# Performance work log

Hardware: AMD Instinct MI355X
Metric: run time of the kernel (lower is better)

## Reference

```python
import jax, jax.numpy as jnp
import numpy as np

B, N, C = 2048, 128, 128
H = 4
NW = 64


def setup_inputs() -> dict:
    key = jax.random.key(0)
    ks = jax.random.split(key, 6)
    return {
        "x": jax.random.normal(ks[0], (B, N, C), dtype=jnp.float32),
        "mask": jax.random.normal(ks[1], (NW, N, N), dtype=jnp.float32),
        "qkv_w": jax.random.normal(ks[2], (3 * C, C), dtype=jnp.float32) * (C ** -0.5),
        "qkv_b": jax.random.normal(ks[3], (3 * C,), dtype=jnp.float32) * 0.02,
        "proj_w": jax.random.normal(ks[4], (C, C), dtype=jnp.float32) * (C ** -0.5),
        "proj_b": jax.random.normal(ks[5], (C,), dtype=jnp.float32) * 0.02,
    }


def reference(x, mask, qkv_w, qkv_b, proj_w, proj_b):
    b, n, c = x.shape
    h = H
    hd = c // h
    scale = hd ** -0.5
    # qkv projection: [B,N,3C] -> [3,B,H,N,hd]
    qkv = (x @ qkv_w.T + qkv_b).reshape(b, n, 3, h, hd).transpose(2, 0, 3, 1, 4)
    q, k, v = qkv[0], qkv[1], qkv[2]
    # scores [B,H,N,N]
    attn = jnp.einsum("bhnd,bhmd->bhnm", q, k) * scale
    nw = mask.shape[0]
    # add per-window mask: view as [B//nW, nW, H, N, N] + mask[None,:,None]
    attn = attn.reshape(b // nw, nw, h, n, n) + mask[None, :, None, :, :]
    attn = attn.reshape(b, h, n, n)
    attn = jax.nn.softmax(attn, axis=-1)
    out = jnp.einsum("bhnm,bhmd->bhnd", attn, v)
    out = out.transpose(0, 2, 1, 3).reshape(b, n, c)
    out = out @ proj_w.T + proj_b
    return out
```

## Files before the change

### kernel.cpp

```cpp
#include <hip/hip_runtime.h>

typedef __bf16 bf16x8 __attribute__((ext_vector_type(8)));
typedef __bf16 bf16x4 __attribute__((ext_vector_type(4)));
typedef float  f32x4  __attribute__((ext_vector_type(4)));

__device__ __forceinline__ int swz(int row, int colb) {
    return row * 256 + (colb ^ ((row & 7) << 4));
}
__device__ __forceinline__ int pswz(int row, int colb) {
    return row * 128 + (colb ^ ((row & 7) << 4));
}

__global__ void prep_weights(const float* __restrict__ qkv_w,
                             const float* __restrict__ proj_w,
                             __bf16* __restrict__ wq, __bf16* __restrict__ wp) {
    int i = blockIdx.x * 256 + threadIdx.x;
    wq[i] = (__bf16)qkv_w[i];
    if (i < 16384) wp[i] = (__bf16)proj_w[i];
}

#define A_LDS_X   0
#define A_LDS_P   0
#define A_LDS_Q   32768
#define A_LDS_K   49152
#define A_LDS_VT  65536
#define A_LDS_TOTAL 81920

__global__ void __launch_bounds__(256, 2)
attn_split(const float* __restrict__ x, const float* __restrict__ mask,
           const float* __restrict__ qkv_b,
           const __bf16* __restrict__ wq,
           __bf16* __restrict__ Og) {
    extern __shared__ char smem[];
    const int b    = blockIdx.x >> 1;
    const int hp   = blockIdx.x & 1;
    const int tid  = threadIdx.x;
    const int wave = tid >> 6;
    const int lane = tid & 63;
    const int l16  = lane & 15;
    const int lg   = lane >> 4;

    {
        const float* xb = x + (size_t)b * 16384;
        #pragma unroll
        for (int it = 0; it < 8; ++it) {
            int i   = it * 256 + tid;
            int row = i >> 4;
            int c8  = (i & 15) << 3;
            float4 f0 = *(const float4*)(xb + row * 128 + c8);
            float4 f1 = *(const float4*)(xb + row * 128 + c8 + 4);
            bf16x8 v;
            v[0] = (__bf16)f0.x; v[1] = (__bf16)f0.y; v[2] = (__bf16)f0.z; v[3] = (__bf16)f0.w;
            v[4] = (__bf16)f1.x; v[5] = (__bf16)f1.y; v[6] = (__bf16)f1.z; v[7] = (__bf16)f1.w;
            *(bf16x8*)(smem + A_LDS_X + swz(row, c8 * 2)) = v;
        }
    }
    __syncthreads();

    const int f0 = wave * 48;
    #pragma unroll
    for (int pass = 0; pass < 2; ++pass) {
        f32x4 acc[3][4];
        #pragma unroll
        for (int jt = 0; jt < 3; ++jt)
            #pragma unroll
            for (int nt = 0; nt < 4; ++nt)
                acc[jt][nt] = {0.f, 0.f, 0.f, 0.f};
        int jg_t[3];
        #pragma unroll
        for (int jt = 0; jt < 3; ++jt) {
            int ft = f0 + jt * 16;
            jg_t[jt] = (ft < 64) ? (hp * 64 + ft)
                     : (ft < 128) ? (128 + hp * 64 + (ft - 64))
                                  : (256 + hp * 64 + (ft - 128));
        }
        #pragma unroll
        for (int kc = 0; kc < 4; ++kc) {
            bf16x8 afr[3];
            #pragma unroll
            for (int jt = 0; jt < 3; ++jt)
                afr[jt] = *(const bf16x8*)(wq + (jg_t[jt] + l16) * 128 + kc * 32 + lg * 8);
            bf16x8 bfr[4];
            #pragma unroll
            for (int nt = 0; nt < 4; ++nt)
                bfr[nt] = *(const bf16x8*)(smem + A_LDS_X +
                            swz((pass * 4 + nt) * 16 + l16, (kc * 32 + lg * 8) * 2));
            #pragma unroll
            for (int jt = 0; jt < 3; ++jt)
                #pragma unroll
                for (int nt = 0; nt < 4; ++nt)
                    acc[jt][nt] = __builtin_amdgcn_mfma_f32_16x16x32_bf16(
                                      afr[jt], bfr[nt], acc[jt][nt], 0, 0, 0);
        }
        #pragma unroll
        for (int jt = 0; jt < 3; ++jt) {
            int ft = f0 + jt * 16;
            int f  = ft + lg * 4;
            float4 bias = *(const float4*)(qkv_b + jg_t[jt] + lg * 4);
            #pragma unroll
            for (int nt = 0; nt < 4; ++nt) {
                int n = (pass * 4 + nt) * 16 + l16;
                f32x4 a = acc[jt][nt];
                __bf16 e0 = (__bf16)(a[0] + bias.x);
                __bf16 e1 = (__bf16)(a[1] + bias.y);
                __bf16 e2 = (__bf16)(a[2] + bias.z);
                __bf16 e3 = (__bf16)(a[3] + bias.w);
                if (f < 64) {
                    bf16x4 v4 = {e0, e1, e2, e3};
                    *(bf16x4*)(smem + A_LDS_Q + pswz(n, f * 2)) = v4;
                } else if (f < 128) {
                    bf16x4 v4 = {e0, e1, e2, e3};
                    *(bf16x4*)(smem + A_LDS_K + pswz(n, (f - 64) * 2)) = v4;
                } else {
                    int d = f - 128;
                    *(__bf16*)(smem + A_LDS_VT + swz(d + 0, n * 2)) = e0;
                    *(__bf16*)(smem + A_LDS_VT + swz(d + 1, n * 2)) = e1;
                    *(__bf16*)(smem + A_LDS_VT + swz(d + 2, n * 2)) = e2;
                    *(__bf16*)(smem + A_LDS_VT + swz(d + 3, n * 2)) = e3;
                }
            }
        }
    }
    __syncthreads();

    const int hl = wave >> 1;
    const int rh = wave & 1;
    const int hgl = hp * 2 + hl;
    const float sc = 0.17677669529663687f;
    bf16x8 kfr[8];
    #pragma unroll
    for (int mt = 0; mt < 8; ++mt)
        kfr[mt] = *(const bf16x8*)(smem + A_LDS_K +
                      pswz(mt * 16 + l16, (hl * 32 + lg * 8) * 2));
    bf16x8 vfr[2][4];
    #pragma unroll
    for (int dt = 0; dt < 2; ++dt)
        #pragma unroll
        for (int kc = 0; kc < 4; ++kc)
            vfr[dt][kc] = *(const bf16x8*)(smem + A_LDS_VT +
                            swz(hl * 32 + dt * 16 + l16, (kc * 32 + lg * 8) * 2));

    const float* mwin = mask + (size_t)(b & 63) * 16384;
    char* pbase = smem + A_LDS_P + wave * 2048;

    #pragma unroll
    for (int i = 0; i < 4; ++i) {
        const int nt = rh * 4 + i;
        bf16x8 qfr = *(const bf16x8*)(smem + A_LDS_Q +
                        pswz(nt * 16 + l16, (hl * 32 + lg * 8) * 2));
        f32x4 s[8];
        #pragma unroll
        for (int mt = 0; mt < 8; ++mt) {
            f32x4 z = {0.f, 0.f, 0.f, 0.f};
            s[mt] = __builtin_amdgcn_mfma_f32_16x16x32_bf16(qfr, kfr[mt], z, 0, 0, 0);
        }
        float mx[4] = {-1e30f, -1e30f, -1e30f, -1e30f};
        #pragma unroll
        for (int mt = 0; mt < 8; ++mt)
            #pragma unroll
            for (int r = 0; r < 4; ++r) {
                float v = s[mt][r] * sc + mwin[(nt * 16 + lg * 4 + r) * 128 + mt * 16 + l16];
                s[mt][r] = v;
                mx[r] = fmaxf(mx[r], v);
            }
        #pragma unroll
        for (int r = 0; r < 4; ++r) {
            float m = mx[r];
            m = fmaxf(m, __shfl_xor(m, 1));
            m = fmaxf(m, __shfl_xor(m, 2));
            m = fmaxf(m, __shfl_xor(m, 4));
            m = fmaxf(m, __shfl_xor(m, 8));
            mx[r] = m;
        }
        float sm[4] = {0.f, 0.f, 0.f, 0.f};
        #pragma unroll
        for (int mt = 0; mt < 8; ++mt)
            #pragma unroll
            for (int r = 0; r < 4; ++r) {
                float p = __expf(s[mt][r] - mx[r]);
                s[mt][r] = p;
                sm[r] += p;
            }
        #pragma unroll
        for (int r = 0; r < 4; ++r) {
            float t = sm[r];
            t += __shfl_xor(t, 1);
            t += __shfl_xor(t, 2);
            t += __shfl_xor(t, 4);
            t += __shfl_xor(t, 8);
            sm[r] = 1.f / t;
        }
        f32x4 o[2];
        o[0] = {0.f, 0.f, 0.f, 0.f};
        o[1] = {0.f, 0.f, 0.f, 0.f};
        #pragma unroll
        for (int hpp = 0; hpp < 2; ++hpp) {
            #pragma unroll
            for (int mtl = 0; mtl < 4; ++mtl) {
                int mt = hpp * 4 + mtl;
                #pragma unroll
                for (int r = 0; r < 4; ++r)
                    *(__bf16*)(pbase + pswz(lg * 4 + r, (mtl * 16 + l16) * 2)) =
                        (__bf16)(s[mt][r] * sm[r]);
            }
            #pragma unroll
            for (int q = 0; q < 2; ++q) {
                int kc = hpp * 2 + q;
                bf16x8 pafr = *(const bf16x8*)(pbase + pswz(l16, (q * 32 + lg * 8) * 2));
                #pragma unroll
                for (int dt = 0; dt < 2; ++dt)
                    o[dt] = __builtin_amdgcn_mfma_f32_16x16x32_bf16(
                                pafr, vfr[dt][kc], o[dt], 0, 0, 0);
            }
        }
        #pragma unroll
        for (int dt = 0; dt < 2; ++dt)
            #pragma unroll
            for (int r = 0; r < 4; ++r)
                Og[((size_t)b * 128 + nt * 16 + lg * 4 + r) * 128 +
                   hgl * 32 + dt * 16 + l16] = (__bf16)o[dt][r];
    }
}

__global__ void __launch_bounds__(256)
proj_out(const __bf16* __restrict__ Og, const __bf16* __restrict__ wp,
         const float* __restrict__ proj_b, float* __restrict__ out) {
    const int b    = blockIdx.x;
    const int tid  = threadIdx.x;
    const int wave = tid >> 6;
    const int l16  = tid & 15;
    const int lg   = (tid & 63) >> 4;

    f32x4 facc[2][8];
    #pragma unroll
    for (int nt2 = 0; nt2 < 2; ++nt2)
        #pragma unroll
        for (int ct = 0; ct < 8; ++ct)
            facc[nt2][ct] = {0.f, 0.f, 0.f, 0.f};
    #pragma unroll
    for (int kc = 0; kc < 4; ++kc) {
        bf16x8 afr[2];
        #pragma unroll
        for (int nt2 = 0; nt2 < 2; ++nt2)
            afr[nt2] = *(const bf16x8*)(Og +
                          ((size_t)b * 128 + wave * 32 + nt2 * 16 + l16) * 128 +
                          kc * 32 + lg * 8);
        bf16x8 bfr[8];
        #pragma unroll
        for (int ct = 0; ct < 8; ++ct)
            bfr[ct] = *(const bf16x8*)(wp + (ct * 16 + l16) * 128 + kc * 32 + lg * 8);
        #pragma unroll
        for (int nt2 = 0; nt2 < 2; ++nt2)
            #pragma unroll
            for (int ct = 0; ct < 8; ++ct)
                facc[nt2][ct] = __builtin_amdgcn_mfma_f32_16x16x32_bf16(
                                    afr[nt2], bfr[ct], facc[nt2][ct], 0, 0, 0);
    }
    float* ob = out + (size_t)b * 16384;
    #pragma unroll
    for (int ct = 0; ct < 8; ++ct) {
        float pb = proj_b[ct * 16 + l16];
        #pragma unroll
        for (int nt2 = 0; nt2 < 2; ++nt2) {
            int n0 = wave * 32 + nt2 * 16 + lg * 4;
            #pragma unroll
            for (int r = 0; r < 4; ++r)
                ob[(n0 + r) * 128 + ct * 16 + l16] = facc[nt2][ct][r] + pb;
        }
    }
}

#define LDS_XO 0
#define LDS_Q  32768
#define LDS_K  65536
#define LDS_VT 98304
#define LDS_P  131072
#define LDS_TOTAL 147456

__global__ void __launch_bounds__(512, 2)
attn_fused(const float* __restrict__ x, const float* __restrict__ mask,
           const float* __restrict__ qkv_b, const float* __restrict__ proj_b,
           const __bf16* __restrict__ wq, const __bf16* __restrict__ wp,
           float* __restrict__ out) {
    extern __shared__ char smem[];
    const int b    = blockIdx.x;
    const int tid  = threadIdx.x;
    const int wave = tid >> 6;
    const int lane = tid & 63;
    const int l16  = lane & 15;
    const int lg   = lane >> 4;

    {
        const float* xb = x + (size_t)b * 16384;
        #pragma unroll
        for (int it = 0; it < 4; ++it) {
            int i   = it * 512 + tid;
            int row = i >> 4;
            int c8  = (i & 15) << 3;
            float4 f0 = *(const float4*)(xb + row * 128 + c8);
            float4 f1 = *(const float4*)(xb + row * 128 + c8 + 4);
            bf16x8 v;
            v[0] = (__bf16)f0.x; v[1] = (__bf16)f0.y; v[2] = (__bf16)f0.z; v[3] = (__bf16)f0.w;
            v[4] = (__bf16)f1.x; v[5] = (__bf16)f1.y; v[6] = (__bf16)f1.z; v[7] = (__bf16)f1.w;
            *(bf16x8*)(smem + LDS_XO + swz(row, c8 * 2)) = v;
        }
    }
    __syncthreads();

    const int j0 = wave * 48;
    #pragma unroll
    for (int pass = 0; pass < 2; ++pass) {
        f32x4 acc[3][4];
        #pragma unroll
        for (int jt = 0; jt < 3; ++jt)
            #pragma unroll
            for (int nt = 0; nt < 4; ++nt)
                acc[jt][nt] = {0.f, 0.f, 0.f, 0.f};
        #pragma unroll
        for (int kc = 0; kc < 4; ++kc) {
            bf16x8 afr[3];
            #pragma unroll
            for (int jt = 0; jt < 3; ++jt)
                afr[jt] = *(const bf16x8*)(wq + (j0 + jt * 16 + l16) * 128 + kc * 32 + lg * 8);
            bf16x8 bfr[4];
            #pragma unroll
            for (int nt = 0; nt < 4; ++nt)
                bfr[nt] = *(const bf16x8*)(smem + LDS_XO +
                            swz((pass * 4 + nt) * 16 + l16, (kc * 32 + lg * 8) * 2));
            #pragma unroll
            for (int jt = 0; jt < 3; ++jt)
                #pragma unroll
                for (int nt = 0; nt < 4; ++nt)
                    acc[jt][nt] = __builtin_amdgcn_mfma_f32_16x16x32_bf16(
                                      afr[jt], bfr[nt], acc[jt][nt], 0, 0, 0);
        }
        #pragma unroll
        for (int jt = 0; jt < 3; ++jt) {
            int jbase = j0 + jt * 16 + lg * 4;
            float4 bias = *(const float4*)(qkv_b + jbase);
            #pragma unroll
            for (int nt = 0; nt < 4; ++nt) {
                int n = (pass * 4 + nt) * 16 + l16;
                f32x4 a = acc[jt][nt];
                __bf16 e0 = (__bf16)(a[0] + bias.x);
                __bf16 e1 = (__bf16)(a[1] + bias.y);
                __bf16 e2 = (__bf16)(a[2] + bias.z);
                __bf16 e3 = (__bf16)(a[3] + bias.w);
                if (jbase < 128) {
                    bf16x4 v4 = {e0, e1, e2, e3};
                    *(bf16x4*)(smem + LDS_Q + swz(n, jbase * 2)) = v4;
                } else if (jbase < 256) {
                    bf16x4 v4 = {e0, e1, e2, e3};
                    *(bf16x4*)(smem + LDS_K + swz(n, (jbase - 128) * 2)) = v4;
                } else {
                    int d = jbase - 256;
                    *(__bf16*)(smem + LDS_VT + swz(d + 0, n * 2)) = e0;
                    *(__bf16*)(smem + LDS_VT + swz(d + 1, n * 2)) = e1;
                    *(__bf16*)(smem + LDS_VT + swz(d + 2, n * 2)) = e2;
                    *(__bf16*)(smem + LDS_VT + swz(d + 3, n * 2)) = e3;
                }
            }
        }
    }
    __syncthreads();

    const int h  = wave >> 1;
    const int rh = wave & 1;
    const float sc = 0.17677669529663687f;
    bf16x8 kfr[8];
    #pragma unroll
    for (int mt = 0; mt < 8; ++mt)
        kfr[mt] = *(const bf16x8*)(smem + LDS_K + swz(mt * 16 + l16, (h * 32 + lg * 8) * 2));
    bf16x8 vfr[2][4];
    #pragma unroll
    for (int dt = 0; dt < 2; ++dt)
        #pragma unroll
        for (int kc = 0; kc < 4; ++kc)
            vfr[dt][kc] = *(const bf16x8*)(smem + LDS_VT +
                            swz(h * 32 + dt * 16 + l16, (kc * 32 + lg * 8) * 2));

    const float* mwin = mask + (size_t)(b & 63) * 16384;
    char* pbase = smem + LDS_P + wave * 2048;

    #pragma unroll
    for (int i = 0; i < 4; ++i) {
        const int nt = rh * 4 + i;
        bf16x8 qfr = *(const bf16x8*)(smem + LDS_Q + swz(nt * 16 + l16, (h * 32 + lg * 8) * 2));
        f32x4 s[8];
        #pragma unroll
        for (int mt = 0; mt < 8; ++mt) {
            f32x4 z = {0.f, 0.f, 0.f, 0.f};
            s[mt] = __builtin_amdgcn_mfma_f32_16x16x32_bf16(qfr, kfr[mt], z, 0, 0, 0);
        }
        float mx[4] = {-1e30f, -1e30f, -1e30f, -1e30f};
        #pragma unroll
        for (int mt = 0; mt < 8; ++mt)
            #pragma unroll
            for (int r = 0; r < 4; ++r) {
                float v = s[mt][r] * sc + mwin[(nt * 16 + lg * 4 + r) * 128 + mt * 16 + l16];
                s[mt][r] = v;
                mx[r] = fmaxf(mx[r], v);
            }
        #pragma unroll
        for (int r = 0; r < 4; ++r) {
            float m = mx[r];
            m = fmaxf(m, __shfl_xor(m, 1));
            m = fmaxf(m, __shfl_xor(m, 2));
            m = fmaxf(m, __shfl_xor(m, 4));
            m = fmaxf(m, __shfl_xor(m, 8));
            mx[r] = m;
        }
        float sm[4] = {0.f, 0.f, 0.f, 0.f};
        #pragma unroll
        for (int mt = 0; mt < 8; ++mt)
            #pragma unroll
            for (int r = 0; r < 4; ++r) {
                float p = __expf(s[mt][r] - mx[r]);
                s[mt][r] = p;
                sm[r] += p;
            }
        #pragma unroll
        for (int r = 0; r < 4; ++r) {
            float t = sm[r];
            t += __shfl_xor(t, 1);
            t += __shfl_xor(t, 2);
            t += __shfl_xor(t, 4);
            t += __shfl_xor(t, 8);
            sm[r] = 1.f / t;
        }
        f32x4 o[2];
        o[0] = {0.f, 0.f, 0.f, 0.f};
        o[1] = {0.f, 0.f, 0.f, 0.f};
        #pragma unroll
        for (int hp2 = 0; hp2 < 2; ++hp2) {
            #pragma unroll
            for (int mtl = 0; mtl < 4; ++mtl) {
                int mt = hp2 * 4 + mtl;
                #pragma unroll
                for (int r = 0; r < 4; ++r)
                    *(__bf16*)(pbase + pswz(lg * 4 + r, (mtl * 16 + l16) * 2)) =
                        (__bf16)(s[mt][r] * sm[r]);
            }
            #pragma unroll
            for (int q = 0; q < 2; ++q) {
                int kc = hp2 * 2 + q;
                bf16x8 pafr = *(const bf16x8*)(pbase + pswz(l16, (q * 32 + lg * 8) * 2));
                #pragma unroll
                for (int dt = 0; dt < 2; ++dt)
                    o[dt] = __builtin_amdgcn_mfma_f32_16x16x32_bf16(
                                pafr, vfr[dt][kc], o[dt], 0, 0, 0);
            }
        }
        #pragma unroll
        for (int dt = 0; dt < 2; ++dt)
            #pragma unroll
            for (int r = 0; r < 4; ++r)
                *(__bf16*)(smem + LDS_XO +
                    swz(nt * 16 + lg * 4 + r, (h * 32 + dt * 16 + l16) * 2)) = (__bf16)o[dt][r];
    }
    __syncthreads();

    f32x4 facc[8];
    #pragma unroll
    for (int ct = 0; ct < 8; ++ct)
        facc[ct] = {0.f, 0.f, 0.f, 0.f};
    #pragma unroll
    for (int kc = 0; kc < 4; ++kc) {
        bf16x8 afr = *(const bf16x8*)(smem + LDS_XO +
                        swz(wave * 16 + l16, (kc * 32 + lg * 8) * 2));
        bf16x8 bfr[8];
        #pragma unroll
        for (int ct = 0; ct < 8; ++ct)
            bfr[ct] = *(const bf16x8*)(wp + (ct * 16 + l16) * 128 + kc * 32 + lg * 8);
        #pragma unroll
        for (int ct = 0; ct < 8; ++ct)
            facc[ct] = __builtin_amdgcn_mfma_f32_16x16x32_bf16(
                           afr, bfr[ct], facc[ct], 0, 0, 0);
    }
    float* ob = out + (size_t)b * 16384;
    #pragma unroll
    for (int ct = 0; ct < 8; ++ct) {
        float pb = proj_b[ct * 16 + l16];
        int n0 = wave * 16 + lg * 4;
        #pragma unroll
        for (int r = 0; r < 4; ++r)
            ob[(n0 + r) * 128 + ct * 16 + l16] = facc[ct][r] + pb;
    }
}

extern "C" void kernel_launch(void* const* d_in, const int* in_sizes, int n_in,
                              void* d_out, int out_size, void* d_ws, size_t ws_size,
                              hipStream_t stream) {
    const float* x      = (const float*)d_in[0];
    const float* mask   = (const float*)d_in[1];
    const float* qkv_w  = (const float*)d_in[2];
    const float* qkv_b  = (const float*)d_in[3];
    const float* proj_w = (const float*)d_in[4];
    const float* proj_b = (const float*)d_in[5];
    float* out = (float*)d_out;

    __bf16* wq = (__bf16*)d_ws;
    __bf16* wp = wq + 49152;

    prep_weights<<<192, 256, 0, stream>>>(qkv_w, proj_w, wq, wp);

    const size_t og_bytes = (size_t)2048 * 128 * 128 * 2;
    const size_t need = 131072 + og_bytes;

    if (ws_size >= need) {
        __bf16* Og = (__bf16*)((char*)d_ws + 131072);
        hipFuncSetAttribute((const void*)attn_split,
                            hipFuncAttributeMaxDynamicSharedMemorySize, A_LDS_TOTAL);
        attn_split<<<4096, 256, A_LDS_TOTAL, stream>>>(x, mask, qkv_b, wq, Og);
        proj_out<<<2048, 256, 0, stream>>>(Og, wp, proj_b, out);
    } else {
        hipFuncSetAttribute((const void*)attn_fused,
                            hipFuncAttributeMaxDynamicSharedMemorySize, LDS_TOTAL);
        attn_fused<<<2048, 512, LDS_TOTAL, stream>>>(x, mask, qkv_b, proj_b, wq, wp, out);
    }
}
```

Measured before the change: 408.5 us.

## Transpose MFMA operands for vectorized mask loads and output stores

Swaps the MFMA operand order in the score, PV and output-projection matmuls so each lane holds four consecutive columns of one row. Mask loads and Og/out stores become float4/bf16x4 accesses, and the row max/sum reductions need two cross-lane shuffles instead of four per row. Softmax normalization moves from the probabilities to the PV output. The probabilities are written to a larger swizzled LDS tile (4096 bytes per wave instead of 2048), and all four PV A-fragments are read up front. This raises per-wave LDS use and changes rounding slightly, since unnormalized probabilities are cast to bf16.

```diff
diff --git a/kernel.cpp b/kernel.cpp
--- a/kernel.cpp
+++ b/kernel.cpp
@@ -141,7 +141,7 @@
                             swz(hl * 32 + dt * 16 + l16, (kc * 32 + lg * 8) * 2));
 
     const float* mwin = mask + (size_t)(b & 63) * 16384;
-    char* pbase = smem + A_LDS_P + wave * 2048;
+    char* pbase = smem + A_LDS_P + wave * 4096;
 
     #pragma unroll
     for (int i = 0; i < 4; ++i) {
@@ -152,73 +152,68 @@
         #pragma unroll
         for (int mt = 0; mt < 8; ++mt) {
             f32x4 z = {0.f, 0.f, 0.f, 0.f};
-            s[mt] = __builtin_amdgcn_mfma_f32_16x16x32_bf16(qfr, kfr[mt], z, 0, 0, 0);
-        }
-        float mx[4] = {-1e30f, -1e30f, -1e30f, -1e30f};
-        #pragma unroll
-        for (int mt = 0; mt < 8; ++mt)
+            s[mt] = __builtin_amdgcn_mfma_f32_16x16x32_bf16(kfr[mt], qfr, z, 0, 0, 0);
+        }
+        const float* mrow = mwin + (size_t)(nt * 16 + l16) * 128;
+        #pragma unroll
+        for (int mt = 0; mt < 8; ++mt) {
+            float4 mk = *(const float4*)(mrow + mt * 16 + lg * 4);
+            s[mt][0] = fmaf(s[mt][0], sc, mk.x);
+            s[mt][1] = fmaf(s[mt][1], sc, mk.y);
+            s[mt][2] = fmaf(s[mt][2], sc, mk.z);
+            s[mt][3] = fmaf(s[mt][3], sc, mk.w);
+        }
+        f32x4 vm0 = s[0], vm1 = s[1];
+        #pragma unroll
+        for (int mt = 2; mt < 8; mt += 2) { 
+            vm0[0]=fmaxf(vm0[0],s[mt][0]); vm0[1]=fmaxf(vm0[1],s[mt][1]);
+            vm0[2]=fmaxf(vm0[2],s[mt][2]); vm0[3]=fmaxf(vm0[3],s[mt][3]);
+            vm1[0]=fmaxf(vm1[0],s[mt+1][0]); vm1[1]=fmaxf(vm1[1],s[mt+1][1]);
+            vm1[2]=fmaxf(vm1[2],s[mt+1][2]); vm1[3]=fmaxf(vm1[3],s[mt+1][3]);
+        }
+        float mx = fmaxf(fmaxf(fmaxf(vm0[0],vm1[0]), fmaxf(vm0[1],vm1[1])),
+                         fmaxf(fmaxf(vm0[2],vm1[2]), fmaxf(vm0[3],vm1[3])));
+        mx = fmaxf(mx, __shfl_xor(mx, 16));
+        mx = fmaxf(mx, __shfl_xor(mx, 32));
+        f32x4 vs = {0.f, 0.f, 0.f, 0.f};
+        #pragma unroll
+        for (int mt = 0; mt < 8; ++mt) {
             #pragma unroll
             for (int r = 0; r < 4; ++r) {
-                float v = s[mt][r] * sc + mwin[(nt * 16 + lg * 4 + r) * 128 + mt * 16 + l16];
-                s[mt][r] = v;
-                mx[r] = fmaxf(mx[r], v);
-            }
-        #pragma unroll
-        for (int r = 0; r < 4; ++r) {
-            float m = mx[r];
-            m = fmaxf(m, __shfl_xor(m, 1));
-            m = fmaxf(m, __shfl_xor(m, 2));
-            m = fmaxf(m, __shfl_xor(m, 4));
-            m = fmaxf(m, __shfl_xor(m, 8));
-            mx[r] = m;
-        }
-        float sm[4] = {0.f, 0.f, 0.f, 0.f};
-        #pragma unroll
-        for (int mt = 0; mt < 8; ++mt)
-            #pragma unroll
-            for (int r = 0; r < 4; ++r) {
-                float p = __expf(s[mt][r] - mx[r]);
+                float p = __expf(s[mt][r] - mx);
                 s[mt][r] = p;
-                sm[r] += p;
-            }
-        #pragma unroll
-        for (int r = 0; r < 4; ++r) {
-            float t = sm[r];
-            t += __shfl_xor(t, 1);
-            t += __shfl_xor(t, 2);
-            t += __shfl_xor(t, 4);
-            t += __shfl_xor(t, 8);
-            sm[r] = 1.f / t;
-        }
+                vs[r] += p;
+            }
+        }
+        float sm = (vs[0] + vs[1]) + (vs[2] + vs[3]);
+        sm += __shfl_xor(sm, 16);
+        sm += __shfl_xor(sm, 32);
+        float inv = 1.f / sm;
+        #pragma unroll
+        for (int mt = 0; mt < 8; ++mt) {
+            bf16x4 pv = {(__bf16)s[mt][0], (__bf16)s[mt][1],
+                         (__bf16)s[mt][2], (__bf16)s[mt][3]};
+            *(bf16x4*)(pbase + swz(l16, mt * 32 + lg * 8)) = pv;
+        }
+        bf16x8 pafr[4];
+        #pragma unroll
+        for (int kc = 0; kc < 4; ++kc)
+            pafr[kc] = *(const bf16x8*)(pbase + swz(l16, kc * 64 + lg * 16));
         f32x4 o[2];
         o[0] = {0.f, 0.f, 0.f, 0.f};
         o[1] = {0.f, 0.f, 0.f, 0.f};
         #pragma unroll
-        for (int hpp = 0; hpp < 2; ++hpp) {
-            #pragma unroll
-            for (int mtl = 0; mtl < 4; ++mtl) {
-                int mt = hpp * 4 + mtl;
-                #pragma unroll
-                for (int r = 0; r < 4; ++r)
-                    *(__bf16*)(pbase + pswz(lg * 4 + r, (mtl * 16 + l16) * 2)) =
-                        (__bf16)(s[mt][r] * sm[r]);
-            }
-            #pragma unroll
-            for (int q = 0; q < 2; ++q) {
-                int kc = hpp * 2 + q;
-                bf16x8 pafr = *(const bf16x8*)(pbase + pswz(l16, (q * 32 + lg * 8) * 2));
-                #pragma unroll
-                for (int dt = 0; dt < 2; ++dt)
-                    o[dt] = __builtin_amdgcn_mfma_f32_16x16x32_bf16(
-                                pafr, vfr[dt][kc], o[dt], 0, 0, 0);
-            }
-        }
-        #pragma unroll
-        for (int dt = 0; dt < 2; ++dt)
-            #pragma unroll
-            for (int r = 0; r < 4; ++r)
-                Og[((size_t)b * 128 + nt * 16 + lg * 4 + r) * 128 +
-                   hgl * 32 + dt * 16 + l16] = (__bf16)o[dt][r];
+        for (int kc = 0; kc < 4; ++kc) {
+            o[0] = __builtin_amdgcn_mfma_f32_16x16x32_bf16(vfr[0][kc], pafr[kc], o[0], 0, 0, 0);
+            o[1] = __builtin_amdgcn_mfma_f32_16x16x32_bf16(vfr[1][kc], pafr[kc], o[1], 0, 0, 0);
+        }
+        __bf16* og = Og + ((size_t)b * 128 + nt * 16 + l16) * 128 + hgl * 32 + lg * 4;
+        #pragma unroll
+        for (int dt = 0; dt < 2; ++dt) {
+            bf16x4 ov = {(__bf16)(o[dt][0] * inv), (__bf16)(o[dt][1] * inv),
+                         (__bf16)(o[dt][2] * inv), (__bf16)(o[dt][3] * inv)};
+            *(bf16x4*)(og + dt * 16) = ov;
+        }
     }
 }
 
@@ -239,33 +234,36 @@
             facc[nt2][ct] = {0.f, 0.f, 0.f, 0.f};
     #pragma unroll
     for (int kc = 0; kc < 4; ++kc) {
-        bf16x8 afr[2];
+        bf16x8 ofr[2];
         #pragma unroll
         for (int nt2 = 0; nt2 < 2; ++nt2)
-            afr[nt2] = *(const bf16x8*)(Og +
+            ofr[nt2] = *(const bf16x8*)(Og +
                           ((size_t)b * 128 + wave * 32 + nt2 * 16 + l16) * 128 +
                           kc * 32 + lg * 8);
-        bf16x8 bfr[8];
+        bf16x8 wfr[8];
         #pragma unroll
         for (int ct = 0; ct < 8; ++ct)
-            bfr[ct] = *(const bf16x8*)(wp + (ct * 16 + l16) * 128 + kc * 32 + lg * 8);
+            wfr[ct] = *(const bf16x8*)(wp + (ct * 16 + l16) * 128 + kc * 32 + lg * 8);
         #pragma unroll
         for (int nt2 = 0; nt2 < 2; ++nt2)
             #pragma unroll
             for (int ct = 0; ct < 8; ++ct)
                 facc[nt2][ct] = __builtin_amdgcn_mfma_f32_16x16x32_bf16(
-                                    afr[nt2], bfr[ct], facc[nt2][ct], 0, 0, 0);
+                                    wfr[ct], ofr[nt2], facc[nt2][ct], 0, 0, 0);
     }
     float* ob = out + (size_t)b * 16384;
     #pragma unroll
     for (int ct = 0; ct < 8; ++ct) {
-        float pb = proj_b[ct * 16 + l16];
+        float4 pb4 = *(const float4*)(proj_b + ct * 16 + lg * 4);
         #pragma unroll
         for (int nt2 = 0; nt2 < 2; ++nt2) {
-            int n0 = wave * 32 + nt2 * 16 + lg * 4;
-            #pragma unroll
-            for (int r = 0; r < 4; ++r)
-                ob[(n0 + r) * 128 + ct * 16 + l16] = facc[nt2][ct][r] + pb;
+            int n = wave * 32 + nt2 * 16 + l16;
+            float4 ov;
+            ov.x = facc[nt2][ct][0] + pb4.x;
+            ov.y = facc[nt2][ct][1] + pb4.y;
+            ov.z = facc[nt2][ct][2] + pb4.z;
+            ov.w = facc[nt2][ct][3] + pb4.w;
+            *(float4*)(ob + n * 128 + ct * 16 + lg * 4) = ov;
         }
     }
 }
```

Result: no change. 406.9 us (-0.4%).
